# Performance work log

Hardware: AMD Instinct MI355X
Metric: run time of the kernel (lower is better)

Reference implementation:

```python
import jax, jax.numpy as jnp
import numpy as np
import math

JOINT_NAMES = ['pelvis', 'hip_R', 'hip_L', 'knee_R', 'knee_L', 'ankle_R', 'ankle_L', 'trunk', 'shoulder_R', 'shoulder_L', 'elbow_R', 'elbow_L']
KINEMATIC_CHAINS = {'pelvis': ['hip_R', 'hip_L', 'trunk'], 'hip_R': ['pelvis', 'knee_R'], 'hip_L': ['pelvis', 'knee_L'], 'knee_R': ['hip_R', 'ankle_R'], 'knee_L': ['hip_L', 'ankle_L'], 'ankle_R': ['knee_R'], 'ankle_L': ['knee_L'], 'trunk': ['pelvis', 'shoulder_R', 'shoulder_L'], 'shoulder_R': ['trunk', 'elbow_R'], 'shoulder_L': ['trunk', 'elbow_L'], 'elbow_R': ['shoulder_R'], 'elbow_L': ['shoulder_L']}

D_MODEL = 128
N_HEADS = 4
HEAD_DIM = D_MODEL // N_HEADS
B = 16384
N = 12

def build_adjacency_matrix():
    n = len(JOINT_NAMES)
    adj = np.zeros((n, n), dtype=np.float32)
    idx = {name: i for i, name in enumerate(JOINT_NAMES)}
    for joint, neighbors in KINEMATIC_CHAINS.items():
        i = idx[joint]
        for nb in neighbors:
            j = idx[nb]
            adj[i, j] = 1.0
            adj[j, i] = 1.0
    adj = adj + np.eye(n, dtype=np.float32)
    return jnp.asarray(adj)

def setup_inputs() -> dict:
    key = jax.random.key(0)
    ks = jax.random.split(key, 12)
    s = 1.0 / math.sqrt(D_MODEL)  # torch Linear default init scale
    inp = {
        'x': jax.random.normal(ks[0], (B, N, D_MODEL), dtype=jnp.float32),
        'visibility': jax.random.uniform(ks[1], (B, N), dtype=jnp.float32),
        'Wq': jax.random.uniform(ks[2], (D_MODEL, D_MODEL), jnp.float32, -s, s),
        'bq': jax.random.uniform(ks[3], (D_MODEL,), jnp.float32, -s, s),
        'Wk': jax.random.uniform(ks[4], (D_MODEL, D_MODEL), jnp.float32, -s, s),
        'bk': jax.random.uniform(ks[5], (D_MODEL,), jnp.float32, -s, s),
        'Wv': jax.random.uniform(ks[6], (D_MODEL, D_MODEL), jnp.float32, -s, s),
        'bv': jax.random.uniform(ks[7], (D_MODEL,), jnp.float32, -s, s),
        'Wo': jax.random.uniform(ks[8], (D_MODEL, D_MODEL), jnp.float32, -s, s),
        'bo': jax.random.uniform(ks[9], (D_MODEL,), jnp.float32, -s, s),
        'bias_scale': jnp.asarray(1.0, dtype=jnp.float32),
        'adjacency': build_adjacency_matrix(),
    }
    return inp

def reference(x, visibility, Wq, bq, Wk, bk, Wv, bv, Wo, bo, bias_scale, adjacency):
    Bsz, Nj, D = x.shape
    # projections; weights stored as (out,in) like torch Linear -> x @ W.T + b
    def proj(W, b):
        return (jnp.einsum('bnd,ed->bne', x, W) + b).reshape(Bsz, Nj, N_HEADS, HEAD_DIM).transpose(0, 2, 1, 3)
    q = proj(Wq, bq)  # (B, H, N, hd)
    k = proj(Wk, bk)
    v = proj(Wv, bv)
    scores = jnp.einsum('bhnd,bhmd->bhnm', q, k) / math.sqrt(HEAD_DIM)
    scores = scores + adjacency[None, None, :, :] * bias_scale
    # visibility mask: subtract 10 where key joint is not visible
    scores = scores - 10.0 * (1.0 - visibility[:, None, None, :])
    attn = jax.nn.softmax(scores, axis=-1)
    out = jnp.einsum('bhnm,bhmd->bhnd', attn, v)
    out = out.transpose(0, 2, 1, 3).reshape(Bsz, Nj, D)
    out = jnp.einsum('bnd,ed->bne', out, Wo) + bo
    return out
```

## Files before the change

kernel.cpp:

```cpp
#include <hip/hip_runtime.h>


typedef unsigned short u16;
typedef short bf16x8 __attribute__((ext_vector_type(8)));
typedef short bf16x4 __attribute__((ext_vector_type(4)));
typedef float f32x4 __attribute__((ext_vector_type(4)));

#define MFMA(a, b, c) __builtin_amdgcn_mfma_f32_16x16x32_bf16((a), (b), (c), 0, 0, 0)

#define BPW   4
#define ROWS  (BPW * 12)
#define XPAD  136
#define VPAD  20
#define PPAD  20

struct SMem {
    u16   qs[ROWS * XPAD];
    u16   ks[ROWS * XPAD];
    u16   vT[BPW * 128 * VPAD];
    u16   P[4 * 16 * PPAD];
    float bias_s[16 * 16];
    float vis_s[BPW * 16];
    float bvec[4 * 128];
    float rls[4 * 16];
};

__device__ __forceinline__ u16 f2b(float f) {
    unsigned u = __builtin_bit_cast(unsigned, f);
    return (u16)((u + 0x7fffu + ((u >> 16) & 1u)) >> 16);
}

__device__ __forceinline__ void st4(u16* p, float a, float b, float c, float d) {
    ushort4 v; v.x = f2b(a); v.y = f2b(b); v.z = f2b(c); v.w = f2b(d);
    *(ushort4*)p = v;
}

__device__ __forceinline__ bf16x8 pack8(float4 a, float4 b) {
    bf16x8 r;
    r[0] = (short)f2b(a.x); r[1] = (short)f2b(a.y);
    r[2] = (short)f2b(a.z); r[3] = (short)f2b(a.w);
    r[4] = (short)f2b(b.x); r[5] = (short)f2b(b.y);
    r[6] = (short)f2b(b.z); r[7] = (short)f2b(b.w);
    return r;
}

__global__ void prep_w(const float* __restrict__ Wq, const float* __restrict__ Wk,
                       const float* __restrict__ Wv, const float* __restrict__ Wo,
                       u16* __restrict__ wbf) {
    int i = blockIdx.x * 256 + threadIdx.x;
    wbf[i]         = f2b(Wq[i]);
    wbf[16384 + i] = f2b(Wk[i]);
    wbf[32768 + i] = f2b(Wv[i]);
    wbf[49152 + i] = f2b(Wo[i]);
}

__global__ __launch_bounds__(256, 3) void cja_main(
    const float* __restrict__ x, const float* __restrict__ vis,
    const float* __restrict__ bq, const float* __restrict__ bk,
    const float* __restrict__ bv, const float* __restrict__ bo,
    const float* __restrict__ bias_scale, const float* __restrict__ adj,
    const u16* __restrict__ wbf, float* __restrict__ out)
{
    extern __shared__ char smraw[];
    SMem& sm = *(SMem*)smraw;

    const int tid  = threadIdx.x;
    const int wave = tid >> 6;
    const int lane = tid & 63;
    const int lq   = lane >> 4;
    const int lm   = lane & 15;
    const int b0   = blockIdx.x * BPW;

    for (int i = tid; i < BPW * 128; i += 256) {
        unsigned* d = (unsigned*)(sm.vT + i * VPAD + 12);
        d[0] = 0u; d[1] = 0u; d[2] = 0u; d[3] = 0u;
    }
    {
        const float L2E = 1.4426950408889634f;
        float scale = bias_scale[0] * L2E;
        int n = tid >> 4, m = tid & 15;
        float bval;
        if (m >= 12)     bval = -1e30f;
        else if (n < 12) bval = adj[n * 12 + m] * scale;
        else             bval = 0.0f;
        sm.bias_s[tid] = bval;
        if (tid < BPW * 16) {
            int bb = tid >> 4, mm = tid & 15;
            sm.vis_s[tid] = (mm < 12) ? 10.0f * L2E * (1.0f - vis[(size_t)(b0 + bb) * 12 + mm])
                                      : 0.0f;
        }
        if (tid < 128) {
            sm.bvec[tid]       = bq[tid];
            sm.bvec[128 + tid] = bk[tid];
            sm.bvec[256 + tid] = bv[tid];
            sm.bvec[384 + tid] = bo[tid];
        }
    }
    __syncthreads();

    {
        const u16* Wq_b = wbf;
        const u16* Wk_b = wbf + 16384;
        const u16* Wv_b = wbf + 32768;
        const float* xw = x + (size_t)b0 * 1536;
        f32x4 accq[2][3], acck[2][3], accv[3][2];
        #pragma unroll
        for (int i = 0; i < 2; i++)
            #pragma unroll
            for (int j = 0; j < 3; j++) { accq[i][j] = (f32x4){0,0,0,0}; acck[i][j] = (f32x4){0,0,0,0}; }
        #pragma unroll
        for (int i = 0; i < 3; i++)
            #pragma unroll
            for (int j = 0; j < 2; j++) accv[i][j] = (f32x4){0,0,0,0};

        const int mrow0 = wave * 32 + lm;
        const int mrow1 = mrow0 + 16;
        #pragma unroll
        for (int ks2 = 0; ks2 < 4; ks2++) {
            const int koff = ks2 * 32 + lq * 8;
            bf16x8 xf[3];
            #pragma unroll
            for (int nt = 0; nt < 3; nt++) {
                const float* xp = xw + (nt * 16 + lm) * 128 + koff;
                float4 u0 = *(const float4*)xp;
                float4 u1 = *(const float4*)(xp + 4);
                xf[nt] = pack8(u0, u1);
            }
            bf16x8 wq0 = *(const bf16x8*)(Wq_b + mrow0 * 128 + koff);
            bf16x8 wq1 = *(const bf16x8*)(Wq_b + mrow1 * 128 + koff);
            bf16x8 wk0 = *(const bf16x8*)(Wk_b + mrow0 * 128 + koff);
            bf16x8 wk1 = *(const bf16x8*)(Wk_b + mrow1 * 128 + koff);
            bf16x8 wv0 = *(const bf16x8*)(Wv_b + mrow0 * 128 + koff);
            bf16x8 wv1 = *(const bf16x8*)(Wv_b + mrow1 * 128 + koff);
            #pragma unroll
            for (int nt = 0; nt < 3; nt++) {
                accq[0][nt] = MFMA(wq0, xf[nt], accq[0][nt]);
                accq[1][nt] = MFMA(wq1, xf[nt], accq[1][nt]);
                acck[0][nt] = MFMA(wk0, xf[nt], acck[0][nt]);
                acck[1][nt] = MFMA(wk1, xf[nt], acck[1][nt]);
                accv[nt][0] = MFMA(xf[nt], wv0, accv[nt][0]);
                accv[nt][1] = MFMA(xf[nt], wv1, accv[nt][1]);
            }
        }
        #pragma unroll
        for (int mi = 0; mi < 2; mi++) {
            const int e0 = (wave * 2 + mi) * 16 + lq * 4;
            float bq0 = sm.bvec[e0], bq1 = sm.bvec[e0+1], bq2 = sm.bvec[e0+2], bq3 = sm.bvec[e0+3];
            float bk0 = sm.bvec[128+e0], bk1 = sm.bvec[128+e0+1], bk2 = sm.bvec[128+e0+2], bk3 = sm.bvec[128+e0+3];
            #pragma unroll
            for (int nt = 0; nt < 3; nt++) {
                const int n = nt * 16 + lm;
                st4(sm.qs + n * XPAD + e0, accq[mi][nt][0]+bq0, accq[mi][nt][1]+bq1,
                                           accq[mi][nt][2]+bq2, accq[mi][nt][3]+bq3);
                st4(sm.ks + n * XPAD + e0, acck[mi][nt][0]+bk0, acck[mi][nt][1]+bk1,
                                           acck[mi][nt][2]+bk2, acck[mi][nt][3]+bk3);
            }
        }
        #pragma unroll
        for (int nt2 = 0; nt2 < 2; nt2++) {
            const int e = (wave * 2 + nt2) * 16 + lm;
            const float bvv = sm.bvec[256 + e];
            #pragma unroll
            for (int mt = 0; mt < 3; mt++) {
                #pragma unroll
                for (int r = 0; r < 4; r++) {
                    int n = mt * 16 + lq * 4 + r;
                    int bb = n / 12, j = n - bb * 12;
                    sm.vT[bb * (128 * VPAD) + e * VPAD + j] = f2b(accv[mt][nt2][r] + bvv);
                }
            }
        }
    }
    __syncthreads();

    {
        const int bl   = wave;
        const int nql  = (lm < 12) ? lm : 11;
        const u16* qrowp = sm.qs + (bl * 12 + nql) * XPAD;
        const u16* krowp = sm.ks + (bl * 12 + nql) * XPAD;
        const float vism = sm.vis_s[bl * 16 + lm];
        float bias_b[4];
        #pragma unroll
        for (int r = 0; r < 4; r++) bias_b[r] = sm.bias_s[(lq * 4 + r) * 16 + lm];
        u16*   Pw  = sm.P + wave * (16 * PPAD);
        float* rlw = sm.rls + wave * 16;
        const u16* vTb = sm.vT + bl * (128 * VPAD);
        const float SC2 = 0.2550348606381560f;
        const bf16x8 z8 = {0,0,0,0,0,0,0,0};
        #pragma unroll
        for (int h = 0; h < 4; h++) {
            bf16x8 qa = *(const bf16x8*)(qrowp + h * 32 + lq * 8);
            bf16x8 kb = *(const bf16x8*)(krowp + h * 32 + lq * 8);
            f32x4 sc = MFMA(qa, kb, ((f32x4){0,0,0,0}));
            #pragma unroll
            for (int r = 0; r < 4; r++) {
                float s2 = sc[r] * SC2 + bias_b[r] - vism;
                float e  = __builtin_amdgcn_exp2f(s2);
                float l  = e;
                l += __shfl_xor(l, 1, 16);
                l += __shfl_xor(l, 2, 16);
                l += __shfl_xor(l, 4, 16);
                l += __shfl_xor(l, 8, 16);
                Pw[(lq * 4 + r) * PPAD + lm] = f2b(e);
                if (lm == 0) rlw[lq * 4 + r] = __builtin_amdgcn_rcpf(l);
            }
            float rln = rlw[lm];
            bf16x8 pb = z8;
            if (lq < 2) {
                const bf16x4* pp = (const bf16x4*)(Pw + lm * PPAD + lq * 8);
                pb = __builtin_shufflevector(pp[0], pp[1], 0, 1, 2, 3, 4, 5, 6, 7);
            }
            #pragma unroll
            for (int mt = 0; mt < 2; mt++) {
                bf16x8 va = z8;
                if (lq < 2) {
                    const bf16x4* vp = (const bf16x4*)(vTb + (h * 32 + mt * 16 + lm) * VPAD + lq * 8);
                    va = __builtin_shufflevector(vp[0], vp[1], 0, 1, 2, 3, 4, 5, 6, 7);
                }
                f32x4 c = MFMA(va, pb, ((f32x4){0,0,0,0}));
                if (lm < 12) {
                    u16* d = sm.qs + (bl * 12 + lm) * XPAD + h * 32 + mt * 16 + lq * 4;
                    st4(d, c[0] * rln, c[1] * rln, c[2] * rln, c[3] * rln);
                }
            }
        }
    }
    __syncthreads();

    {
        const u16* Wo_b = wbf + 49152;
        f32x4 acc[2][3];
        #pragma unroll
        for (int i = 0; i < 2; i++)
            #pragma unroll
            for (int j = 0; j < 3; j++) acc[i][j] = (f32x4){0,0,0,0};
        const int m0 = wave * 32 + lm;
        #pragma unroll
        for (int ks2 = 0; ks2 < 4; ks2++) {
            const int koff = ks2 * 32 + lq * 8;
            bf16x8 a0 = *(const bf16x8*)(Wo_b + m0 * 128 + koff);
            bf16x8 a1 = *(const bf16x8*)(Wo_b + (m0 + 16) * 128 + koff);
            #pragma unroll
            for (int nt = 0; nt < 3; nt++) {
                bf16x8 bfr = *(const bf16x8*)(sm.qs + (nt * 16 + lm) * XPAD + koff);
                acc[0][nt] = MFMA(a0, bfr, acc[0][nt]);
                acc[1][nt] = MFMA(a1, bfr, acc[1][nt]);
            }
        }
        #pragma unroll
        for (int mi = 0; mi < 2; mi++) {
            const int e0 = (wave * 2 + mi) * 16 + lq * 4;
            float bo0 = sm.bvec[384+e0], bo1 = sm.bvec[384+e0+1],
                  bo2 = sm.bvec[384+e0+2], bo3 = sm.bvec[384+e0+3];
            #pragma unroll
            for (int nt = 0; nt < 3; nt++) {
                const int n = nt * 16 + lm;
                float4 o;
                o.x = acc[mi][nt][0] + bo0;
                o.y = acc[mi][nt][1] + bo1;
                o.z = acc[mi][nt][2] + bo2;
                o.w = acc[mi][nt][3] + bo3;
                *(float4*)(out + ((size_t)(b0 * 12 + n) << 7) + e0) = o;
            }
        }
    }
}

extern "C" void kernel_launch(void* const* d_in, const int* in_sizes, int n_in,
                              void* d_out, int out_size, void* d_ws, size_t ws_size,
                              hipStream_t stream) {
    const float* x   = (const float*)d_in[0];
    const float* vis = (const float*)d_in[1];
    const float* Wq  = (const float*)d_in[2];
    const float* bq  = (const float*)d_in[3];
    const float* Wk  = (const float*)d_in[4];
    const float* bk  = (const float*)d_in[5];
    const float* Wv  = (const float*)d_in[6];
    const float* bv  = (const float*)d_in[7];
    const float* Wo  = (const float*)d_in[8];
    const float* bo  = (const float*)d_in[9];
    const float* bs  = (const float*)d_in[10];
    const float* adj = (const float*)d_in[11];
    u16* wbf = (u16*)d_ws;

    prep_w<<<64, 256, 0, stream>>>(Wq, Wk, Wv, Wo, wbf);
    cja_main<<<16384 / BPW, 256, sizeof(SMem), stream>>>(
        x, vis, bq, bk, bv, bo, bs, adj, wbf, (float*)d_out);
}
```

Baseline: 288.2 us.

## Persistent grid with async LDS prefetch of pre-converted bf16 x tiles

```diff
diff --git a/kernel.cpp b/kernel.cpp
--- a/kernel.cpp
+++ b/kernel.cpp
@@ -13,6 +13,10 @@
 #define XPAD  136
 #define VPAD  20
 #define PPAD  20
+#define NGRP  4096
+#define GRID  768
+#define XS_BYTES (ROWS * XPAD * 2)
+#define XS_CHUNKS 13
 
 struct SMem {
     u16   qs[ROWS * XPAD];
@@ -20,7 +24,6 @@
     u16   vT[BPW * 128 * VPAD];
     u16   P[4 * 16 * PPAD];
     float bias_s[16 * 16];
-    float vis_s[BPW * 16];
     float bvec[4 * 128];
     float rls[4 * 16];
 };
@@ -42,6 +45,19 @@
     r[4] = (short)f2b(b.x); r[5] = (short)f2b(b.y);
     r[6] = (short)f2b(b.z); r[7] = (short)f2b(b.w);
     return r;
+}
+
+__device__ __forceinline__ void stage16(const u16* g, u16* l) {
+    __builtin_amdgcn_global_load_lds(
+        (const __attribute__((address_space(1))) void*)g,
+        (__attribute__((address_space(3))) void*)l, 16, 0, 0);
+}
+
+__device__ __forceinline__ void bar_lgkm() {
+    asm volatile("s_waitcnt lgkmcnt(0)" ::: "memory");
+    __builtin_amdgcn_sched_barrier(0);
+    __builtin_amdgcn_s_barrier();
+    __builtin_amdgcn_sched_barrier(0);
 }
 
 __global__ void prep_w(const float* __restrict__ Wq, const float* __restrict__ Wk,
@@ -54,8 +70,17 @@
     wbf[49152 + i] = f2b(Wo[i]);
 }
 
+__global__ void prep_x(const float* __restrict__ x, u16* __restrict__ xbf) {
+    size_t i = ((size_t)blockIdx.x * 256 + threadIdx.x) * 8;
+    float4 a = *(const float4*)(x + i);
+    float4 b = *(const float4*)(x + i + 4);
+    *(bf16x8*)(xbf + i) = pack8(a, b);
+}
+
+template <bool STAGE>
 __global__ __launch_bounds__(256, 3) void cja_main(
-    const float* __restrict__ x, const float* __restrict__ vis,
+    const float* __restrict__ x, const u16* __restrict__ xbf,
+    const float* __restrict__ vis,
     const float* __restrict__ bq, const float* __restrict__ bk,
     const float* __restrict__ bv, const float* __restrict__ bo,
     const float* __restrict__ bias_scale, const float* __restrict__ adj,
@@ -69,14 +94,35 @@
     const int lane = tid & 63;
     const int lq   = lane >> 4;
     const int lm   = lane & 15;
-    const int b0   = blockIdx.x * BPW;
-
-    for (int i = tid; i < BPW * 128; i += 256) {
+
+    u16* xs = (u16*)sm.vT;
+
+    int srcoff[4];
+    #pragma unroll
+    for (int i = 0; i < 4; i++) {
+        int ci  = wave + i * 4;
+        int p   = ci * 512 + lane * 8;
+        int row = p / 136; if (row > 47) row = 47;
+        int col = (p - row * 136) & 127;
+        srcoff[i] = row * 128 + col;
+    }
+    auto issue_stage = [&](int grp) {
+        const u16* gb = xbf + (size_t)grp * (ROWS * 128);
+        #pragma unroll
+        for (int i = 0; i < 4; i++) {
+            int ci = wave + i * 4;
+            if (ci < XS_CHUNKS) stage16(gb + srcoff[i], xs + ci * 512);
+        }
+    };
+
+    if constexpr (STAGE) issue_stage(blockIdx.x);
+
+    for (int i = 333 + tid; i < BPW * 128; i += 256) {
         unsigned* d = (unsigned*)(sm.vT + i * VPAD + 12);
         d[0] = 0u; d[1] = 0u; d[2] = 0u; d[3] = 0u;
     }
+    const float L2E = 1.4426950408889634f;
     {
-        const float L2E = 1.4426950408889634f;
         float scale = bias_scale[0] * L2E;
         int n = tid >> 4, m = tid & 15;
         float bval;
@@ -84,11 +130,6 @@
         else if (n < 12) bval = adj[n * 12 + m] * scale;
         else             bval = 0.0f;
         sm.bias_s[tid] = bval;
-        if (tid < BPW * 16) {
-            int bb = tid >> 4, mm = tid & 15;
-            sm.vis_s[tid] = (mm < 12) ? 10.0f * L2E * (1.0f - vis[(size_t)(b0 + bb) * 12 + mm])
-                                      : 0.0f;
-        }
         if (tid < 128) {
             sm.bvec[tid]       = bq[tid];
             sm.bvec[128 + tid] = bk[tid];
@@ -98,171 +139,192 @@
     }
     __syncthreads();
 
-    {
-        const u16* Wq_b = wbf;
-        const u16* Wk_b = wbf + 16384;
-        const u16* Wv_b = wbf + 32768;
-        const float* xw = x + (size_t)b0 * 1536;
-        f32x4 accq[2][3], acck[2][3], accv[3][2];
-        #pragma unroll
-        for (int i = 0; i < 2; i++)
-            #pragma unroll
-            for (int j = 0; j < 3; j++) { accq[i][j] = (f32x4){0,0,0,0}; acck[i][j] = (f32x4){0,0,0,0}; }
-        #pragma unroll
-        for (int i = 0; i < 3; i++)
-            #pragma unroll
-            for (int j = 0; j < 2; j++) accv[i][j] = (f32x4){0,0,0,0};
-
-        const int mrow0 = wave * 32 + lm;
-        const int mrow1 = mrow0 + 16;
-        #pragma unroll
-        for (int ks2 = 0; ks2 < 4; ks2++) {
-            const int koff = ks2 * 32 + lq * 8;
-            bf16x8 xf[3];
-            #pragma unroll
-            for (int nt = 0; nt < 3; nt++) {
-                const float* xp = xw + (nt * 16 + lm) * 128 + koff;
-                float4 u0 = *(const float4*)xp;
-                float4 u1 = *(const float4*)(xp + 4);
-                xf[nt] = pack8(u0, u1);
-            }
-            bf16x8 wq0 = *(const bf16x8*)(Wq_b + mrow0 * 128 + koff);
-            bf16x8 wq1 = *(const bf16x8*)(Wq_b + mrow1 * 128 + koff);
-            bf16x8 wk0 = *(const bf16x8*)(Wk_b + mrow0 * 128 + koff);
-            bf16x8 wk1 = *(const bf16x8*)(Wk_b + mrow1 * 128 + koff);
-            bf16x8 wv0 = *(const bf16x8*)(Wv_b + mrow0 * 128 + koff);
-            bf16x8 wv1 = *(const bf16x8*)(Wv_b + mrow1 * 128 + koff);
-            #pragma unroll
-            for (int nt = 0; nt < 3; nt++) {
-                accq[0][nt] = MFMA(wq0, xf[nt], accq[0][nt]);
-                accq[1][nt] = MFMA(wq1, xf[nt], accq[1][nt]);
-                acck[0][nt] = MFMA(wk0, xf[nt], acck[0][nt]);
-                acck[1][nt] = MFMA(wk1, xf[nt], acck[1][nt]);
-                accv[nt][0] = MFMA(xf[nt], wv0, accv[nt][0]);
-                accv[nt][1] = MFMA(xf[nt], wv1, accv[nt][1]);
-            }
-        }
-        #pragma unroll
-        for (int mi = 0; mi < 2; mi++) {
-            const int e0 = (wave * 2 + mi) * 16 + lq * 4;
-            float bq0 = sm.bvec[e0], bq1 = sm.bvec[e0+1], bq2 = sm.bvec[e0+2], bq3 = sm.bvec[e0+3];
-            float bk0 = sm.bvec[128+e0], bk1 = sm.bvec[128+e0+1], bk2 = sm.bvec[128+e0+2], bk3 = sm.bvec[128+e0+3];
-            #pragma unroll
-            for (int nt = 0; nt < 3; nt++) {
-                const int n = nt * 16 + lm;
-                st4(sm.qs + n * XPAD + e0, accq[mi][nt][0]+bq0, accq[mi][nt][1]+bq1,
-                                           accq[mi][nt][2]+bq2, accq[mi][nt][3]+bq3);
-                st4(sm.ks + n * XPAD + e0, acck[mi][nt][0]+bk0, acck[mi][nt][1]+bk1,
-                                           acck[mi][nt][2]+bk2, acck[mi][nt][3]+bk3);
-            }
-        }
-        #pragma unroll
-        for (int nt2 = 0; nt2 < 2; nt2++) {
-            const int e = (wave * 2 + nt2) * 16 + lm;
-            const float bvv = sm.bvec[256 + e];
-            #pragma unroll
-            for (int mt = 0; mt < 3; mt++) {
+    const int bl  = wave;
+    const int nql = (lm < 12) ? lm : 11;
+    const u16* qrowp = sm.qs + (bl * 12 + nql) * XPAD;
+    const u16* krowp = sm.ks + (bl * 12 + nql) * XPAD;
+    u16*   Pw  = sm.P + wave * (16 * PPAD);
+    float* rlw = sm.rls + wave * 16;
+    const u16* vTb = sm.vT + bl * (128 * VPAD);
+    const int mrow0 = wave * 32 + lm;
+    const int mrow1 = mrow0 + 16;
+    float bias_b[4];
+    #pragma unroll
+    for (int rr = 0; rr < 4; rr++) bias_b[rr] = sm.bias_s[(lq * 4 + rr) * 16 + lm];
+
+    #pragma unroll 1
+    for (int grp = blockIdx.x; grp < NGRP; grp += GRID) {
+        const int  b0      = grp * BPW;
+        const bool hasNext = (grp + GRID) < NGRP;
+
+        float vism;
+        {
+            int   j  = (lm < 12) ? lm : 0;
+            float vr = vis[(size_t)(b0 + bl) * 12 + j];
+            vism = (lm < 12) ? 10.0f * L2E * (1.0f - vr) : 0.0f;
+        }
+
+        {
+            const u16* Wq_b = wbf;
+            const u16* Wk_b = wbf + 16384;
+            const u16* Wv_b = wbf + 32768;
+            f32x4 accq[2][3], acck[2][3], accv[3][2];
+            #pragma unroll
+            for (int i = 0; i < 2; i++)
+                #pragma unroll
+                for (int j = 0; j < 3; j++) { accq[i][j] = (f32x4){0,0,0,0}; acck[i][j] = (f32x4){0,0,0,0}; }
+            #pragma unroll
+            for (int i = 0; i < 3; i++)
+                #pragma unroll
+                for (int j = 0; j < 2; j++) accv[i][j] = (f32x4){0,0,0,0};
+            #pragma unroll
+            for (int ks2 = 0; ks2 < 4; ks2++) {
+                const int koff = ks2 * 32 + lq * 8;
+                bf16x8 xt[3];
+                if constexpr (STAGE) {
+                    #pragma unroll
+                    for (int nt = 0; nt < 3; nt++)
+                        xt[nt] = *(const bf16x8*)(xs + (nt * 16 + lm) * XPAD + koff);
+                } else {
+                    const float* xw = x + (size_t)b0 * 1536;
+                    #pragma unroll
+                    for (int nt = 0; nt < 3; nt++) {
+                        const float* xp = xw + (nt * 16 + lm) * 128 + koff;
+                        float4 u0 = *(const float4*)xp;
+                        float4 u1 = *(const float4*)(xp + 4);
+                        xt[nt] = pack8(u0, u1);
+                    }
+                }
+                bf16x8 wq0 = *(const bf16x8*)(Wq_b + mrow0 * 128 + koff);
+                bf16x8 wq1 = *(const bf16x8*)(Wq_b + mrow1 * 128 + koff);
+                bf16x8 wk0 = *(const bf16x8*)(Wk_b + mrow0 * 128 + koff);
+                bf16x8 wk1 = *(const bf16x8*)(Wk_b + mrow1 * 128 + koff);
+                bf16x8 wv0 = *(const bf16x8*)(Wv_b + mrow0 * 128 + koff);
+                bf16x8 wv1 = *(const bf16x8*)(Wv_b + mrow1 * 128 + koff);
+                #pragma unroll
+                for (int nt = 0; nt < 3; nt++) {
+                    accq[0][nt] = MFMA(wq0, xt[nt], accq[0][nt]);
+                    accq[1][nt] = MFMA(wq1, xt[nt], accq[1][nt]);
+                    acck[0][nt] = MFMA(wk0, xt[nt], acck[0][nt]);
+                    acck[1][nt] = MFMA(wk1, xt[nt], acck[1][nt]);
+                    accv[nt][0] = MFMA(xt[nt], wv0, accv[nt][0]);
+                    accv[nt][1] = MFMA(xt[nt], wv1, accv[nt][1]);
+                }
+            }
+            #pragma unroll
+            for (int mi = 0; mi < 2; mi++) {
+                const int e0 = (wave * 2 + mi) * 16 + lq * 4;
+                float bq0 = sm.bvec[e0], bq1 = sm.bvec[e0+1], bq2 = sm.bvec[e0+2], bq3 = sm.bvec[e0+3];
+                float bk0 = sm.bvec[128+e0], bk1 = sm.bvec[128+e0+1], bk2 = sm.bvec[128+e0+2], bk3 = sm.bvec[128+e0+3];
+                #pragma unroll
+                for (int nt = 0; nt < 3; nt++) {
+                    const int n = nt * 16 + lm;
+                    st4(sm.qs + n * XPAD + e0, accq[mi][nt][0]+bq0, accq[mi][nt][1]+bq1,
+                                               accq[mi][nt][2]+bq2, accq[mi][nt][3]+bq3);
+                    st4(sm.ks + n * XPAD + e0, acck[mi][nt][0]+bk0, acck[mi][nt][1]+bk1,
+                                               acck[mi][nt][2]+bk2, acck[mi][nt][3]+bk3);
+                }
+            }
+            bar_lgkm();
+            #pragma unroll
+            for (int nt2 = 0; nt2 < 2; nt2++) {
+                const int e = (wave * 2 + nt2) * 16 + lm;
+                const float bvv = sm.bvec[256 + e];
+                #pragma unroll
+                for (int mt = 0; mt < 3; mt++) {
+                    #pragma unroll
+                    for (int r = 0; r < 4; r++) {
+                        int n = mt * 16 + lq * 4 + r;
+                        int bb = n / 12, j = n - bb * 12;
+                        sm.vT[bb * (128 * VPAD) + e * VPAD + j] = f2b(accv[mt][nt2][r] + bvv);
+                    }
+                }
+            }
+        }
+        bar_lgkm();
+
+        {
+            const float SC2 = 0.2550348606381560f;
+            const bf16x8 z8 = {0,0,0,0,0,0,0,0};
+            #pragma unroll
+            for (int h = 0; h < 4; h++) {
+                bf16x8 qa = *(const bf16x8*)(qrowp + h * 32 + lq * 8);
+                bf16x8 kb = *(const bf16x8*)(krowp + h * 32 + lq * 8);
+                f32x4 sc = MFMA(qa, kb, ((f32x4){0,0,0,0}));
                 #pragma unroll
                 for (int r = 0; r < 4; r++) {
-                    int n = mt * 16 + lq * 4 + r;
-                    int bb = n / 12, j = n - bb * 12;
-                    sm.vT[bb * (128 * VPAD) + e * VPAD + j] = f2b(accv[mt][nt2][r] + bvv);
-                }
-            }
-        }
-    }
-    __syncthreads();
-
-    {
-        const int bl   = wave;
-        const int nql  = (lm < 12) ? lm : 11;
-        const u16* qrowp = sm.qs + (bl * 12 + nql) * XPAD;
-        const u16* krowp = sm.ks + (bl * 12 + nql) * XPAD;
-        const float vism = sm.vis_s[bl * 16 + lm];
-        float bias_b[4];
-        #pragma unroll
-        for (int r = 0; r < 4; r++) bias_b[r] = sm.bias_s[(lq * 4 + r) * 16 + lm];
-        u16*   Pw  = sm.P + wave * (16 * PPAD);
-        float* rlw = sm.rls + wave * 16;
-        const u16* vTb = sm.vT + bl * (128 * VPAD);
-        const float SC2 = 0.2550348606381560f;
-        const bf16x8 z8 = {0,0,0,0,0,0,0,0};
-        #pragma unroll
-        for (int h = 0; h < 4; h++) {
-            bf16x8 qa = *(const bf16x8*)(qrowp + h * 32 + lq * 8);
-            bf16x8 kb = *(const bf16x8*)(krowp + h * 32 + lq * 8);
-            f32x4 sc = MFMA(qa, kb, ((f32x4){0,0,0,0}));
-            #pragma unroll
-            for (int r = 0; r < 4; r++) {
-                float s2 = sc[r] * SC2 + bias_b[r] - vism;
-                float e  = __builtin_amdgcn_exp2f(s2);
-                float l  = e;
-                l += __shfl_xor(l, 1, 16);
-                l += __shfl_xor(l, 2, 16);
-                l += __shfl_xor(l, 4, 16);
-                l += __shfl_xor(l, 8, 16);
-                Pw[(lq * 4 + r) * PPAD + lm] = f2b(e);
-                if (lm == 0) rlw[lq * 4 + r] = __builtin_amdgcn_rcpf(l);
-            }
-            float rln = rlw[lm];
-            bf16x8 pb = z8;
-            if (lq < 2) {
-                const bf16x4* pp = (const bf16x4*)(Pw + lm * PPAD + lq * 8);
-                pb = __builtin_shufflevector(pp[0], pp[1], 0, 1, 2, 3, 4, 5, 6, 7);
-            }
-            #pragma unroll
-            for (int mt = 0; mt < 2; mt++) {
-                bf16x8 va = z8;
+                    float s2 = sc[r] * SC2 + bias_b[r] - vism;
+                    float e  = __builtin_amdgcn_exp2f(s2);
+                    float l  = e;
+                    l += __shfl_xor(l, 1, 16);
+                    l += __shfl_xor(l, 2, 16);
+                    l += __shfl_xor(l, 4, 16);
+                    l += __shfl_xor(l, 8, 16);
+                    Pw[(lq * 4 + r) * PPAD + lm] = f2b(e);
+                    if (lm == 0) rlw[lq * 4 + r] = __builtin_amdgcn_rcpf(l);
+                }
+                float rln = rlw[lm];
+                bf16x8 pb = z8;
                 if (lq < 2) {
-                    const bf16x4* vp = (const bf16x4*)(vTb + (h * 32 + mt * 16 + lm) * VPAD + lq * 8);
-                    va = __builtin_shufflevector(vp[0], vp[1], 0, 1, 2, 3, 4, 5, 6, 7);
-                }
-                f32x4 c = MFMA(va, pb, ((f32x4){0,0,0,0}));
-                if (lm < 12) {
-                    u16* d = sm.qs + (bl * 12 + lm) * XPAD + h * 32 + mt * 16 + lq * 4;
-                    st4(d, c[0] * rln, c[1] * rln, c[2] * rln, c[3] * rln);
-                }
-            }
-        }
-    }
-    __syncthreads();
-
-    {
-        const u16* Wo_b = wbf + 49152;
-        f32x4 acc[2][3];
-        #pragma unroll
-        for (int i = 0; i < 2; i++)
-            #pragma unroll
-            for (int j = 0; j < 3; j++) acc[i][j] = (f32x4){0,0,0,0};
-        const int m0 = wave * 32 + lm;
-        #pragma unroll
-        for (int ks2 = 0; ks2 < 4; ks2++) {
-            const int koff = ks2 * 32 + lq * 8;
-            bf16x8 a0 = *(const bf16x8*)(Wo_b + m0 * 128 + koff);
-            bf16x8 a1 = *(const bf16x8*)(Wo_b + (m0 + 16) * 128 + koff);
-            #pragma unroll
-            for (int nt = 0; nt < 3; nt++) {
-                bf16x8 bfr = *(const bf16x8*)(sm.qs + (nt * 16 + lm) * XPAD + koff);
-                acc[0][nt] = MFMA(a0, bfr, acc[0][nt]);
-                acc[1][nt] = MFMA(a1, bfr, acc[1][nt]);
-            }
-        }
-        #pragma unroll
-        for (int mi = 0; mi < 2; mi++) {
-            const int e0 = (wave * 2 + mi) * 16 + lq * 4;
-            float bo0 = sm.bvec[384+e0], bo1 = sm.bvec[384+e0+1],
-                  bo2 = sm.bvec[384+e0+2], bo3 = sm.bvec[384+e0+3];
-            #pragma unroll
-            for (int nt = 0; nt < 3; nt++) {
-                const int n = nt * 16 + lm;
-                float4 o;
-                o.x = acc[mi][nt][0] + bo0;
-                o.y = acc[mi][nt][1] + bo1;
-                o.z = acc[mi][nt][2] + bo2;
-                o.w = acc[mi][nt][3] + bo3;
-                *(float4*)(out + ((size_t)(b0 * 12 + n) << 7) + e0) = o;
-            }
-        }
+                    const bf16x4* pp = (const bf16x4*)(Pw + lm * PPAD + lq * 8);
+                    pb = __builtin_shufflevector(pp[0], pp[1], 0, 1, 2, 3, 4, 5, 6, 7);
+                }
+                #pragma unroll
+                for (int mt = 0; mt < 2; mt++) {
+                    bf16x8 va = z8;
+                    if (lq < 2) {
+                        const bf16x4* vp2 = (const bf16x4*)(vTb + (h * 32 + mt * 16 + lm) * VPAD + lq * 8);
+                        va = __builtin_shufflevector(vp2[0], vp2[1], 0, 1, 2, 3, 4, 5, 6, 7);
+                    }
+                    f32x4 c = MFMA(va, pb, ((f32x4){0,0,0,0}));
+                    if (lm < 12) {
+                        u16* d = sm.qs + (bl * 12 + lm) * XPAD + h * 32 + mt * 16 + lq * 4;
+                        st4(d, c[0] * rln, c[1] * rln, c[2] * rln, c[3] * rln);
+                    }
+                }
+            }
+        }
+        bar_lgkm();
+
+        {
+            if constexpr (STAGE) { if (hasNext) issue_stage(grp + GRID); }
+
+            const u16* Wo_b = wbf + 49152;
+            f32x4 acc[2][3];
+            #pragma unroll
+            for (int i = 0; i < 2; i++)
+                #pragma unroll
+                for (int j = 0; j < 3; j++) acc[i][j] = (f32x4){0,0,0,0};
+            #pragma unroll
+            for (int ks2 = 0; ks2 < 4; ks2++) {
+                const int koff = ks2 * 32 + lq * 8;
+                bf16x8 a0 = *(const bf16x8*)(Wo_b + mrow0 * 128 + koff);
+                bf16x8 a1 = *(const bf16x8*)(Wo_b + mrow1 * 128 + koff);
+                #pragma unroll
+                for (int nt = 0; nt < 3; nt++) {
+                    bf16x8 bfr = *(const bf16x8*)(sm.qs + (nt * 16 + lm) * XPAD + koff);
+                    acc[0][nt] = MFMA(a0, bfr, acc[0][nt]);
+                    acc[1][nt] = MFMA(a1, bfr, acc[1][nt]);
+                }
+            }
+            #pragma unroll
+            for (int mi = 0; mi < 2; mi++) {
+                const int e0 = (wave * 2 + mi) * 16 + lq * 4;
+                float bo0 = sm.bvec[384+e0], bo1 = sm.bvec[384+e0+1],
+                      bo2 = sm.bvec[384+e0+2], bo3 = sm.bvec[384+e0+3];
+                #pragma unroll
+                for (int nt = 0; nt < 3; nt++) {
+                    const int n = nt * 16 + lm;
+                    float4 o;
+                    o.x = acc[mi][nt][0] + bo0;
+                    o.y = acc[mi][nt][1] + bo1;
+                    o.z = acc[mi][nt][2] + bo2;
+                    o.w = acc[mi][nt][3] + bo3;
+                    *(float4*)(out + ((size_t)(b0 * 12 + n) << 7) + e0) = o;
+                }
+            }
+        }
+        if (hasNext) __syncthreads();
     }
 }
 
@@ -282,8 +344,17 @@
     const float* bs  = (const float*)d_in[10];
     const float* adj = (const float*)d_in[11];
     u16* wbf = (u16*)d_ws;
+    u16* xbf = wbf + 65536;
+
+    const size_t need = 131072 + (size_t)16384 * 12 * 128 * 2;
 
     prep_w<<<64, 256, 0, stream>>>(Wq, Wk, Wv, Wo, wbf);
-    cja_main<<<16384 / BPW, 256, sizeof(SMem), stream>>>(
-        x, vis, bq, bk, bv, bo, bs, adj, wbf, (float*)d_out);
-}
+    if (ws_size >= need) {
+        prep_x<<<12288, 256, 0, stream>>>(x, xbf);
+        cja_main<true><<<GRID, 256, sizeof(SMem), stream>>>(
+            x, xbf, vis, bq, bk, bv, bo, bs, adj, wbf, (float*)d_out);
+    } else {
+        cja_main<false><<<GRID, 256, sizeof(SMem), stream>>>(
+            x, xbf, vis, bq, bk, bv, bo, bs, adj, wbf, (float*)d_out);
+    }
+}
```

Result: slower. 316.5 us (+9.8%).
